# Kernel optimization log

Measured on AMD Instinct MI355X. Metric: run time of the kernel, lower is better.

Reference implementation:

```python
import jax, jax.numpy as jnp
import numpy as np

B, T, N_EMBED, HEADSIZE = 16, 2048, 1024, 128


def setup_inputs() -> dict:
    key = jax.random.key(0)
    kx, kq, kk, kv = jax.random.split(key, 4)
    x = jax.random.normal(kx, (B, T, N_EMBED), dtype=jnp.float32)
    # nn.Linear(n_embed, headsize, bias=False): y = x @ W, W stored [n_embed, headsize]
    s = (1.0 / np.sqrt(N_EMBED)).astype(np.float32)
    Wq = jax.random.normal(kq, (N_EMBED, HEADSIZE), dtype=jnp.float32) * s
    Wk = jax.random.normal(kk, (N_EMBED, HEADSIZE), dtype=jnp.float32) * s
    Wv = jax.random.normal(kv, (N_EMBED, HEADSIZE), dtype=jnp.float32) * s
    return {"x": x, "Wq": Wq, "Wk": Wk, "Wv": Wv}


def reference(x, Wq, Wk, Wv):
    Bsz, Tlen, C = x.shape
    q = x @ Wq  # [B, T, H]
    k = x @ Wk  # [B, T, H]
    v = x @ Wv  # [B, T, H]
    scale = C ** (-0.5)  # NOTE: original scales by n_embed**-0.5, not headsize**-0.5
    wt = jnp.einsum('bqh,bkh->bqk', q, k) * scale  # [B, T, T]
    causal = jnp.tril(jnp.ones((Tlen, Tlen), dtype=bool))
    wt = jnp.where(causal, wt, -jnp.inf)
    wt = jax.nn.softmax(wt, axis=-1)
    # dropout is identity in eval mode
    out = jnp.einsum('bqk,bkh->bqh', wt, v)  # [B, T, H]
    return out
```

## Files before the change

### kernel.cpp

```cpp
#include <hip/hip_runtime.h>
#include <hip/hip_bf16.h>

#define BATCH 16
#define TLEN 2048
#define CDIM 1024
#define HDIM 128

typedef __attribute__((ext_vector_type(8))) short bf16x8;
typedef __attribute__((ext_vector_type(4))) float f32x4;
typedef __attribute__((ext_vector_type(16))) float f32x16;
typedef __attribute__((ext_vector_type(4))) unsigned short u16x4;
typedef __attribute__((ext_vector_type(8))) unsigned short u16x8;

static __device__ __forceinline__ unsigned short f2bf(float f) {
    __hip_bfloat16 h = __float2bfloat16(f);
    return *(unsigned short*)&h;
}
static __device__ __forceinline__ unsigned pkbf(float a, float b) {
    return (unsigned)f2bf(a) | ((unsigned)f2bf(b) << 16);
}
static __device__ __forceinline__ int part_offs(int qc) {
    const int g = qc >> 2;
    return qc + 2 * g * (g - 1) + (qc & 3) * g;
}

typedef const __attribute__((address_space(1))) unsigned int* gas_t;
typedef __attribute__((address_space(3))) unsigned int* las_t;
static __device__ __forceinline__ void gl_lds16(const void* g, void* l) {
    __builtin_amdgcn_global_load_lds((gas_t)g, (las_t)l, 16, 0, 0);
}

static __device__ __forceinline__ void hard_barrier() {
    __builtin_amdgcn_sched_barrier(0);
    __builtin_amdgcn_s_barrier();
    __builtin_amdgcn_sched_barrier(0);
}

__global__ __launch_bounds__(256) void pack_w(
    const float* __restrict__ Wq, const float* __restrict__ Wk,
    const float* __restrict__ Wv, unsigned short* __restrict__ wtb)
{
    const int which = blockIdx.y;
    const float* W = (which == 0) ? Wq : (which == 1) ? Wk : Wv;
    const int n = blockIdx.x >> 2;
    const int k = (blockIdx.x & 3) * 256 + threadIdx.x;
    wtb[((size_t)which * 128 + n) * 1024 + k] = f2bf(W[(size_t)k * 128 + n]);
}

__global__ __launch_bounds__(512, 2) void qkv_fused(
    const float* __restrict__ x, const unsigned short* __restrict__ wtb,
    unsigned short* __restrict__ qb, unsigned short* __restrict__ kb,
    unsigned short* __restrict__ vtb)
{
    __shared__ __align__(16) unsigned short Ab[2][256 * 64];
    __shared__ __align__(16) unsigned short Bb[2][192 * 64];

    const int xcd = blockIdx.x & 7, s = blockIdx.x >> 3;
    const int m0 = (xcd * 16 + (s >> 1)) * 256;
    const int nh = s & 1;

    const int tid  = threadIdx.x;
    const int lane = tid & 63, wid = tid >> 6;
    const int wm = wid >> 2, wn = wid & 3;
    const int c = lane & 15, g = lane >> 4;

    const int arow = tid >> 1, ah = tid & 1;
    const float* xsrc = x + (size_t)(m0 + arow) * CDIM + ah * 32;

    f32x4 acc[8][3];
#pragma unroll
    for (int i = 0; i < 8; ++i)
#pragma unroll
        for (int j = 0; j < 3; ++j) acc[i][j] = (f32x4){0.f, 0.f, 0.f, 0.f};

    float4 As0, As1, As2, As3, As4, As5, As6, As7;

#define AISSUE(k0_)                                                          \
    { const float* s_ = xsrc + (k0_);                                        \
      As0 = *(const float4*)(s_);       As1 = *(const float4*)(s_ + 4);      \
      As2 = *(const float4*)(s_ + 8);   As3 = *(const float4*)(s_ + 12);     \
      As4 = *(const float4*)(s_ + 16);  As5 = *(const float4*)(s_ + 20);     \
      As6 = *(const float4*)(s_ + 24);  As7 = *(const float4*)(s_ + 28); }

#define CVT2(lo_, hi_, dst_)                                                 \
    { u16x8 t_;                                                              \
      t_[0]=f2bf(lo_.x); t_[1]=f2bf(lo_.y); t_[2]=f2bf(lo_.z); t_[3]=f2bf(lo_.w); \
      t_[4]=f2bf(hi_.x); t_[5]=f2bf(hi_.y); t_[6]=f2bf(hi_.z); t_[7]=f2bf(hi_.w); \
      *(u16x8*)(dst_) = t_; }

#define AWRITE(bi_)                                                          \
    { char* ba_ = (char*)Ab[bi_] + arow * 128;                               \
      const int sw_ = (arow & 7) << 4;                                       \
      CVT2(As0, As1, ba_ + ((ah * 64 +  0) ^ sw_));                          \
      CVT2(As2, As3, ba_ + ((ah * 64 + 16) ^ sw_));                          \
      CVT2(As4, As5, ba_ + ((ah * 64 + 32) ^ sw_));                          \
      CVT2(As6, As7, ba_ + ((ah * 64 + 48) ^ sw_)); }

#define BISSUE(k0_, bi_)                                                     \
    { _Pragma("unroll")                                                      \
      for (int i_ = 0; i_ < 3; ++i_) {                                       \
          const int seg_ = wid * 3 + i_;                                     \
          const int row_ = seg_ * 8 + (lane >> 3);                           \
          const int gr_  = (lane & 7) ^ (row_ & 7);                          \
          gl_lds16(wtb + (size_t)(nh * 192 + row_) * 1024 + (k0_) + gr_ * 8, \
                   (char*)Bb[bi_] + seg_ * 1024);                            \
      } }

    AISSUE(0);
    BISSUE(0, 0);
    asm volatile("s_waitcnt vmcnt(3)" ::: "memory");
    AWRITE(0);
    asm volatile("s_waitcnt vmcnt(0) lgkmcnt(0)" ::: "memory");
    hard_barrier();

#pragma unroll 1
    for (int kt = 0; kt < 16; ++kt) {
        const int cur = kt & 1;
        if (kt < 15) {
            AISSUE((kt + 1) * 64);
            BISSUE((kt + 1) * 64, cur ^ 1);
        }

#pragma unroll
        for (int ks = 0; ks < 2; ++ks) {
            bf16x8 af[8], bf[3];
#pragma unroll
            for (int mf = 0; mf < 8; ++mf) {
                const int rm = wm * 128 + mf * 16 + c;
                af[mf] = *(const bf16x8*)((char*)Ab[cur] + rm * 128 +
                                          ((ks * 64 + g * 16) ^ ((rm & 7) << 4)));
            }
#pragma unroll
            for (int nf = 0; nf < 3; ++nf) {
                const int rn = wn * 48 + nf * 16 + c;
                bf[nf] = *(const bf16x8*)((char*)Bb[cur] + rn * 128 +
                                          ((ks * 64 + g * 16) ^ ((rn & 7) << 4)));
            }
            __builtin_amdgcn_s_setprio(1);
#pragma unroll
            for (int mf = 0; mf < 8; ++mf)
#pragma unroll
                for (int nf = 0; nf < 3; ++nf)
                    acc[mf][nf] = __builtin_amdgcn_mfma_f32_16x16x32_bf16(
                        af[mf], bf[nf], acc[mf][nf], 0, 0, 0);
            __builtin_amdgcn_s_setprio(0);
        }

        if (kt < 15) {
            asm volatile("s_waitcnt vmcnt(3)" ::: "memory");
            AWRITE(cur ^ 1);
            asm volatile("s_waitcnt vmcnt(0) lgkmcnt(0)" ::: "memory");
            hard_barrier();
        }
    }

#pragma unroll
    for (int mf = 0; mf < 8; ++mf) {
#pragma unroll
        for (int nf = 0; nf < 3; ++nf) {
            const int col0 = nh * 192 + wn * 48 + nf * 16;
            const int nt = col0 >> 7;
            const int nc = (col0 & 127) + c;
            const int m = m0 + wm * 128 + mf * 16 + g * 4;
            if (nt == 0) {
#pragma unroll
                for (int r = 0; r < 4; ++r)
                    qb[(size_t)(m + r) * HDIM + nc] = f2bf(acc[mf][nf][r] * 0.03125f);
            } else if (nt == 1) {
#pragma unroll
                for (int r = 0; r < 4; ++r)
                    kb[(size_t)(m + r) * HDIM + nc] = f2bf(acc[mf][nf][r]);
            } else {
                const int b = m >> 11, tl = m & (TLEN - 1);
                u16x4 o;
                o[0] = f2bf(acc[mf][nf][0]); o[1] = f2bf(acc[mf][nf][1]);
                o[2] = f2bf(acc[mf][nf][2]); o[3] = f2bf(acc[mf][nf][3]);
                *(u16x4*)(vtb + ((size_t)b * HDIM + nc) * TLEN + tl) = o;
            }
        }
    }
#undef AISSUE
#undef CVT2
#undef AWRITE
#undef BISSUE
}

__global__ __launch_bounds__(256, 2) void attn_partial(
    const short* __restrict__ qb, const short* __restrict__ kb,
    const short* __restrict__ vtb,
    unsigned short* __restrict__ Opart, float* __restrict__ mpart,
    float* __restrict__ lpart)
{
    const int kc = blockIdx.x;
    const int qc = blockIdx.y;
    const int b  = blockIdx.z;
    if (kc > (qc >> 2)) return;
    const int kv_base = kc * 512;
    const int qrel = qc * 128 - kv_base;
    int NT = (qrel >> 6) + 2; if (NT > 8) NT = 8;

    __shared__ unsigned short Ks[2][64 * 128];
    __shared__ unsigned short Vs[2][128 * 64];

    const int tid  = threadIdx.x;
    const int wid  = tid >> 6;
    const int lane = tid & 63;
    const int c5 = lane & 31, hi = lane >> 5;
    const int q0w = qc * 128 + wid * 32;
    const int qg  = q0w + c5;
    const int pidx = b * 40 + part_offs(qc) + kc;

    const short* Kb  = kb  + (size_t)b * TLEN * HDIM;
    const short* Vtb = vtb + (size_t)b * HDIM * TLEN;

    bf16x8 qf[8];
#pragma unroll
    for (int ks = 0; ks < 8; ++ks)
        qf[ks] = *(const bf16x8*)(qb + ((size_t)b * TLEN + qg) * HDIM + ks * 16 + hi * 8);

    bf16x8 kst[4], vst[4];

#define GLOAD(kv0_)                                                          \
    {                                                                        \
        _Pragma("unroll")                                                    \
        for (int it = 0; it < 4; ++it) {                                     \
            const int o = tid * 16 + it * 4096;                              \
            const int kr = o >> 8, kcb = o & 0xF0;                           \
            kst[it] = *(const bf16x8*)((const char*)Kb +                     \
                        (size_t)((kv0_) + kr) * 256 + kcb);                  \
            const int vr = o >> 7, vcb = o & 0x70;                           \
            vst[it] = *(const bf16x8*)((const char*)Vtb +                    \
                        (size_t)vr * (TLEN * 2) + (size_t)(kv0_) * 2 + vcb); \
        }                                                                    \
    }
#define SSTORE(bi_)                                                          \
    {                                                                        \
        _Pragma("unroll")                                                    \
        for (int it = 0; it < 4; ++it) {                                     \
            const int o = tid * 16 + it * 4096;                              \
            const int kr = o >> 8, kcb = o & 0xF0;                           \
            *(bf16x8*)((char*)Ks[bi_] + kr * 256 + (kcb ^ ((kr & 7) << 4))) = kst[it]; \
            const int vr = o >> 7, vcb = o & 0x70;                           \
            *(bf16x8*)((char*)Vs[bi_] + vr * 128 + (vcb ^ ((vr & 7) << 4))) = vst[it]; \
        }                                                                    \
    }

    GLOAD(kv_base);
    SSTORE(0);
    __syncthreads();

    f32x16 oacc[4];
#pragma unroll
    for (int i = 0; i < 4; ++i)
#pragma unroll
        for (int r = 0; r < 16; ++r) oacc[i][r] = 0.f;
    float m_r = -1e30f;
    float l_r = 0.f;

#pragma unroll 1
    for (int t = 0; t < NT; ++t) {
        const int bi = t & 1;
        if (t + 1 < NT) GLOAD(kv_base + 64 * (t + 1));

        const int kv0 = kv_base + 64 * t;
        if (kv0 <= q0w + 31) {
            f32x16 s0, s1;
#pragma unroll
            for (int r = 0; r < 16; ++r) { s0[r] = 0.f; s1[r] = 0.f; }
            __builtin_amdgcn_s_setprio(1);
#pragma unroll
            for (int ks = 0; ks < 8; ++ks) {
                const int col = ks * 32 + hi * 16;
                const int off0 = c5 * 256 + (col ^ ((c5 & 7) << 4));
                const int off1 = (32 + c5) * 256 + (col ^ ((c5 & 7) << 4));
                bf16x8 a0 = *(const bf16x8*)((char*)Ks[bi] + off0);
                bf16x8 a1 = *(const bf16x8*)((char*)Ks[bi] + off1);
                s0 = __builtin_amdgcn_mfma_f32_32x32x16_bf16(a0, qf[ks], s0, 0, 0, 0);
                s1 = __builtin_amdgcn_mfma_f32_32x32x16_bf16(a1, qf[ks], s1, 0, 0, 0);
            }
            __builtin_amdgcn_s_setprio(0);

            if (kv0 + 63 > q0w) {
#pragma unroll
                for (int r = 0; r < 16; ++r) {
                    const int key0 = kv0 + (r & 3) + 8 * (r >> 2) + 4 * hi;
                    if (key0 > qg)      s0[r] = -INFINITY;
                    if (key0 + 32 > qg) s1[r] = -INFINITY;
                }
            }

            float t8[8];
#pragma unroll
            for (int i = 0; i < 8; ++i)
                t8[i] = fmaxf(fmaxf(s0[2*i], s0[2*i+1]), fmaxf(s1[2*i], s1[2*i+1]));
            float smax = fmaxf(fmaxf(fmaxf(t8[0], t8[1]), fmaxf(t8[2], t8[3])),
                               fmaxf(fmaxf(t8[4], t8[5]), fmaxf(t8[6], t8[7])));
            smax = fmaxf(smax, __shfl_xor(smax, 32));

            const bool defer = __all(smax - m_r <= 8.0f);
            const float mnew = defer ? m_r : fmaxf(m_r, smax);
            if (!defer) {
                const float alpha = __expf(m_r - mnew);
                l_r *= alpha;
#pragma unroll
                for (int hb = 0; hb < 4; ++hb) oacc[hb] = oacc[hb] * alpha;
            }
            m_r = mnew;

#pragma unroll
            for (int r = 0; r < 16; ++r) {
                s0[r] = __expf(s0[r] - mnew);
                s1[r] = __expf(s1[r] - mnew);
            }
            float a8[8];
#pragma unroll
            for (int i = 0; i < 8; ++i)
                a8[i] = (s0[2*i] + s0[2*i+1]) + (s1[2*i] + s1[2*i+1]);
            float psum = ((a8[0] + a8[1]) + (a8[2] + a8[3])) +
                         ((a8[4] + a8[5]) + (a8[6] + a8[7]));
            psum += __shfl_xor(psum, 32);
            l_r += psum;

            bf16x8 pa[4];
#pragma unroll
            for (int kb2 = 0; kb2 < 2; ++kb2) {
#pragma unroll
                for (int par = 0; par < 2; ++par) {
                    const int e = par * 8;
                    float v0, v1, v2, v3, v4, v5, v6, v7;
                    if (kb2 == 0) {
                        v0=s0[e+0]; v1=s0[e+1]; v2=s0[e+2]; v3=s0[e+3];
                        v4=s0[e+4]; v5=s0[e+5]; v6=s0[e+6]; v7=s0[e+7];
                    } else {
                        v0=s1[e+0]; v1=s1[e+1]; v2=s1[e+2]; v3=s1[e+3];
                        v4=s1[e+4]; v5=s1[e+5]; v6=s1[e+6]; v7=s1[e+7];
                    }
                    const unsigned w0 = pkbf(v0, v1), w1 = pkbf(v2, v3);
                    const unsigned w2 = pkbf(v4, v5), w3 = pkbf(v6, v7);
                    const unsigned X0 = hi ? w0 : w2;
                    const unsigned X1 = hi ? w1 : w3;
                    const unsigned R0 = (unsigned)__shfl_xor((int)X0, 32);
                    const unsigned R1 = (unsigned)__shfl_xor((int)X1, 32);
                    union { unsigned w[4]; bf16x8 v; } uu;
                    uu.w[0] = hi ? R0 : w0;  uu.w[1] = hi ? R1 : w1;
                    uu.w[2] = hi ? w2 : R0;  uu.w[3] = hi ? w3 : R1;
                    pa[kb2 * 2 + par] = uu.v;
                }
            }

            __builtin_amdgcn_s_setprio(1);
#pragma unroll
            for (int hb = 0; hb < 4; ++hb) {
                const int row = hb * 32 + c5;
#pragma unroll
                for (int ks = 0; ks < 4; ++ks) {
                    const int off = row * 128 + ((ks * 32 + hi * 16) ^ ((row & 7) << 4));
                    bf16x8 va = *(const bf16x8*)((char*)Vs[bi] + off);
                    oacc[hb] = __builtin_amdgcn_mfma_f32_32x32x16_bf16(va, pa[ks], oacc[hb], 0, 0, 0);
                }
            }
            __builtin_amdgcn_s_setprio(0);
        }

        if (t + 1 < NT) {
            SSTORE(bi ^ 1);
            __syncthreads();
        }
    }

    __syncthreads();
    char* sl = (char*)Ks + wid * 8192;
#pragma unroll
    for (int hb = 0; hb < 4; ++hb)
#pragma unroll
        for (int rq = 0; rq < 4; ++rq) {
            u16x4 o4;
            o4[0] = f2bf(oacc[hb][rq * 4 + 0]);
            o4[1] = f2bf(oacc[hb][rq * 4 + 1]);
            o4[2] = f2bf(oacc[hb][rq * 4 + 2]);
            o4[3] = f2bf(oacc[hb][rq * 4 + 3]);
            const int off = c5 * 256 + ((hb * 64 + rq * 16 + hi * 8) ^ ((c5 & 7) << 4));
            *(u16x4*)(sl + off) = o4;
        }
    asm volatile("s_waitcnt lgkmcnt(0)" ::: "memory");
    __builtin_amdgcn_sched_barrier(0);

    const int qr = lane >> 1, hf = lane & 1;
    unsigned short* Og = Opart + (size_t)pidx * 128 * 128 +
                         (size_t)(wid * 32 + qr) * 128 + hf * 64;
#pragma unroll
    for (int i = 0; i < 8; ++i) {
        const int off = qr * 256 + ((hf * 128 + i * 16) ^ ((qr & 7) << 4));
        *(u16x8*)(Og + i * 8) = *(const u16x8*)(sl + off);
    }
    if (hi == 0) {
        mpart[(size_t)pidx * 128 + wid * 32 + c5] = m_r;
        lpart[(size_t)pidx * 128 + wid * 32 + c5] = l_r;
    }
#undef GLOAD
#undef SSTORE
}

__global__ __launch_bounds__(256) void attn_combine(
    const unsigned short* __restrict__ Opart, const float* __restrict__ mpart,
    const float* __restrict__ lpart, float* __restrict__ out)
{
    const int qc = blockIdx.x;
    const int b  = blockIdx.y;
    const int n  = (qc >> 2) + 1;
    const int base = b * 40 + part_offs(qc);
    const int t   = threadIdx.x;
    const int row = t >> 1;
    const int d0  = (t & 1) * 64;

    float mv[4], lv[4];
#pragma unroll
    for (int p = 0; p < 4; ++p) {
        mv[p] = (p < n) ? mpart[(size_t)(base + p) * 128 + row] : -INFINITY;
        lv[p] = (p < n) ? lpart[(size_t)(base + p) * 128 + row] : 0.f;
    }
    float M = fmaxf(fmaxf(mv[0], mv[1]), fmaxf(mv[2], mv[3]));
    float L = 0.f;
    float wv[4];
#pragma unroll
    for (int p = 0; p < 4; ++p) {
        wv[p] = (p < n) ? __expf(mv[p] - M) : 0.f;
        L += wv[p] * lv[p];
    }

    float acc[64];
#pragma unroll
    for (int i = 0; i < 64; ++i) acc[i] = 0.f;

    for (int p = 0; p < n; ++p) {
        const float w = wv[p];
        const bf16x8* src = (const bf16x8*)(Opart +
            ((size_t)(base + p) * 128 + row) * 128 + d0);
#pragma unroll
        for (int j = 0; j < 8; ++j) {
            bf16x8 v = src[j];
#pragma unroll
            for (int e = 0; e < 8; ++e) {
                union { unsigned u; float f; } xx;
                xx.u = ((unsigned)(unsigned short)v[e]) << 16;
                acc[j * 8 + e] += w * xx.f;
            }
        }
    }

    const float invL = 1.f / L;
    float4* dst = (float4*)(out + ((size_t)(b * TLEN + qc * 128 + row)) * 128 + d0);
#pragma unroll
    for (int i = 0; i < 16; ++i)
        dst[i] = make_float4(acc[4*i] * invL, acc[4*i+1] * invL,
                             acc[4*i+2] * invL, acc[4*i+3] * invL);
}

extern "C" void kernel_launch(void* const* d_in, const int* in_sizes, int n_in,
                              void* d_out, int out_size, void* d_ws, size_t ws_size,
                              hipStream_t stream)
{
    const float* x  = (const float*)d_in[0];
    const float* Wq = (const float*)d_in[1];
    const float* Wk = (const float*)d_in[2];
    const float* Wv = (const float*)d_in[3];
    float* outp = (float*)d_out;

    const size_t per = (size_t)BATCH * TLEN * HDIM;
    unsigned short* qb  = (unsigned short*)d_ws;
    unsigned short* kb  = qb + per;
    unsigned short* vtb = kb + per;
    unsigned short* wtb = vtb + per;
    unsigned short* Opart = wtb + 384 * 1024;
    float* mpart = (float*)(Opart + (size_t)640 * 128 * 128);
    float* lpart = mpart + (size_t)640 * 128;

    dim3 gw(512, 3);
    pack_w<<<gw, 256, 0, stream>>>(Wq, Wk, Wv, wtb);

    qkv_fused<<<256, 512, 0, stream>>>(x, wtb, qb, kb, vtb);

    dim3 g2(4, 16, BATCH);
    attn_partial<<<g2, 256, 0, stream>>>((const short*)qb, (const short*)kb,
                                         (const short*)vtb, Opart, mpart, lpart);

    dim3 g3(16, BATCH);
    attn_combine<<<g3, 256, 0, stream>>>(Opart, mpart, lpart, outp);
}
```

Before: 136.8 us.

## Retile QKV GEMM to 128-row blocks with 32x32 MFMA and LDS-transposed weight pack

The QKV projection kernel now uses 256-thread blocks covering 128 rows instead of 512-thread blocks covering 256 rows, doubling the grid to 512 blocks. Each wave computes a 64x96 tile with 32x32x16 bf16 MFMAs instead of 16x16x32, which needs fewer fragment loads per FLOP. The weight pack kernel transposes through LDS with coalesced float4 reads and 16-byte writes instead of strided scalar accesses. Smaller M tiles mean each block reloads the weight tile for less reused work, and the epilogue issues more scattered stores.

```diff
diff --git a/kernel.cpp b/kernel.cpp
--- a/kernel.cpp
+++ b/kernel.cpp
@@ -42,36 +42,61 @@
 {
     const int which = blockIdx.y;
     const float* W = (which == 0) ? Wq : (which == 1) ? Wk : Wv;
-    const int n = blockIdx.x >> 2;
-    const int k = (blockIdx.x & 3) * 256 + threadIdx.x;
-    wtb[((size_t)which * 128 + n) * 1024 + k] = f2bf(W[(size_t)k * 128 + n]);
-}
-
-__global__ __launch_bounds__(512, 2) void qkv_fused(
+    const int k0 = blockIdx.x * 64;
+
+    __shared__ float T[64][132];
+
+    const int tid = threadIdx.x;
+#pragma unroll
+    for (int i = 0; i < 8; ++i) {
+        const int e = tid + i * 256;
+        const int row = e >> 5, c4 = e & 31;
+        float4 v = *(const float4*)(W + (size_t)(k0 + row) * 128 + c4 * 4);
+        T[row][c4 * 4 + 0] = v.x; T[row][c4 * 4 + 1] = v.y;
+        T[row][c4 * 4 + 2] = v.z; T[row][c4 * 4 + 3] = v.w;
+    }
+    __syncthreads();
+
+    const int n  = tid >> 1;
+    const int kh = (tid & 1) * 32;
+    unsigned short* dst = wtb + ((size_t)which * 128 + n) * 1024 + k0 + kh;
+#pragma unroll
+    for (int j = 0; j < 4; ++j) {
+        u16x8 o;
+#pragma unroll
+        for (int e2 = 0; e2 < 8; ++e2)
+            o[e2] = f2bf(T[kh + j * 8 + e2][n]);
+        *(u16x8*)(dst + j * 8) = o;
+    }
+}
+
+__global__ __launch_bounds__(256, 2) void qkv_fused(
     const float* __restrict__ x, const unsigned short* __restrict__ wtb,
     unsigned short* __restrict__ qb, unsigned short* __restrict__ kb,
     unsigned short* __restrict__ vtb)
 {
-    __shared__ __align__(16) unsigned short Ab[2][256 * 64];
+    __shared__ __align__(16) unsigned short Ab[2][128 * 64];
     __shared__ __align__(16) unsigned short Bb[2][192 * 64];
 
     const int xcd = blockIdx.x & 7, s = blockIdx.x >> 3;
-    const int m0 = (xcd * 16 + (s >> 1)) * 256;
+    const int m0 = (xcd * 32 + (s >> 1)) * 128;
     const int nh = s & 1;
 
     const int tid  = threadIdx.x;
     const int lane = tid & 63, wid = tid >> 6;
-    const int wm = wid >> 2, wn = wid & 3;
-    const int c = lane & 15, g = lane >> 4;
+    const int wm = wid >> 1, wn = wid & 1;
+    const int c5 = lane & 31, hi = lane >> 5;
 
     const int arow = tid >> 1, ah = tid & 1;
     const float* xsrc = x + (size_t)(m0 + arow) * CDIM + ah * 32;
 
-    f32x4 acc[8][3];
-#pragma unroll
-    for (int i = 0; i < 8; ++i)
-#pragma unroll
-        for (int j = 0; j < 3; ++j) acc[i][j] = (f32x4){0.f, 0.f, 0.f, 0.f};
+    f32x16 acc[2][3];
+#pragma unroll
+    for (int i = 0; i < 2; ++i)
+#pragma unroll
+        for (int j = 0; j < 3; ++j)
+#pragma unroll
+            for (int r = 0; r < 16; ++r) acc[i][j][r] = 0.f;
 
     float4 As0, As1, As2, As3, As4, As5, As6, As7;
 
@@ -98,8 +123,8 @@
 
 #define BISSUE(k0_, bi_)                                                     \
     { _Pragma("unroll")                                                      \
-      for (int i_ = 0; i_ < 3; ++i_) {                                       \
-          const int seg_ = wid * 3 + i_;                                     \
+      for (int i_ = 0; i_ < 6; ++i_) {                                       \
+          const int seg_ = wid * 6 + i_;                                     \
           const int row_ = seg_ * 8 + (lane >> 3);                           \
           const int gr_  = (lane & 7) ^ (row_ & 7);                          \
           gl_lds16(wtb + (size_t)(nh * 192 + row_) * 1024 + (k0_) + gr_ * 8, \
@@ -108,7 +133,7 @@
 
     AISSUE(0);
     BISSUE(0, 0);
-    asm volatile("s_waitcnt vmcnt(3)" ::: "memory");
+    asm volatile("s_waitcnt vmcnt(6)" ::: "memory");
     AWRITE(0);
     asm volatile("s_waitcnt vmcnt(0) lgkmcnt(0)" ::: "memory");
     hard_barrier();
@@ -122,32 +147,32 @@
         }
 
 #pragma unroll
-        for (int ks = 0; ks < 2; ++ks) {
-            bf16x8 af[8], bf[3];
-#pragma unroll
-            for (int mf = 0; mf < 8; ++mf) {
-                const int rm = wm * 128 + mf * 16 + c;
-                af[mf] = *(const bf16x8*)((char*)Ab[cur] + rm * 128 +
-                                          ((ks * 64 + g * 16) ^ ((rm & 7) << 4)));
-            }
-#pragma unroll
-            for (int nf = 0; nf < 3; ++nf) {
-                const int rn = wn * 48 + nf * 16 + c;
-                bf[nf] = *(const bf16x8*)((char*)Bb[cur] + rn * 128 +
-                                          ((ks * 64 + g * 16) ^ ((rn & 7) << 4)));
+        for (int kk = 0; kk < 4; ++kk) {
+            bf16x8 af[2], bf[3];
+#pragma unroll
+            for (int tm = 0; tm < 2; ++tm) {
+                const int rm = wm * 64 + tm * 32 + c5;
+                af[tm] = *(const bf16x8*)((char*)Ab[cur] + rm * 128 +
+                                          ((kk * 32 + hi * 16) ^ ((rm & 7) << 4)));
+            }
+#pragma unroll
+            for (int tn = 0; tn < 3; ++tn) {
+                const int rn = wn * 96 + tn * 32 + c5;
+                bf[tn] = *(const bf16x8*)((char*)Bb[cur] + rn * 128 +
+                                          ((kk * 32 + hi * 16) ^ ((rn & 7) << 4)));
             }
             __builtin_amdgcn_s_setprio(1);
 #pragma unroll
-            for (int mf = 0; mf < 8; ++mf)
-#pragma unroll
-                for (int nf = 0; nf < 3; ++nf)
-                    acc[mf][nf] = __builtin_amdgcn_mfma_f32_16x16x32_bf16(
-                        af[mf], bf[nf], acc[mf][nf], 0, 0, 0);
+            for (int tm = 0; tm < 2; ++tm)
+#pragma unroll
+                for (int tn = 0; tn < 3; ++tn)
+                    acc[tm][tn] = __builtin_amdgcn_mfma_f32_32x32x16_bf16(
+                        af[tm], bf[tn], acc[tm][tn], 0, 0, 0);
             __builtin_amdgcn_s_setprio(0);
         }
 
         if (kt < 15) {
-            asm volatile("s_waitcnt vmcnt(3)" ::: "memory");
+            asm volatile("s_waitcnt vmcnt(6)" ::: "memory");
             AWRITE(cur ^ 1);
             asm volatile("s_waitcnt vmcnt(0) lgkmcnt(0)" ::: "memory");
             hard_barrier();
@@ -155,27 +180,39 @@
     }
 
 #pragma unroll
-    for (int mf = 0; mf < 8; ++mf) {
-#pragma unroll
-        for (int nf = 0; nf < 3; ++nf) {
-            const int col0 = nh * 192 + wn * 48 + nf * 16;
-            const int nt = col0 >> 7;
-            const int nc = (col0 & 127) + c;
-            const int m = m0 + wm * 128 + mf * 16 + g * 4;
+    for (int tm = 0; tm < 2; ++tm) {
+#pragma unroll
+        for (int tn = 0; tn < 3; ++tn) {
+            const int colg = nh * 192 + wn * 96 + tn * 32;
+            const int nt = colg >> 7;
+            const int nc = (colg & 127) + c5;
+            const int mb2 = m0 + wm * 64 + tm * 32 + 4 * hi;
             if (nt == 0) {
 #pragma unroll
-                for (int r = 0; r < 4; ++r)
-                    qb[(size_t)(m + r) * HDIM + nc] = f2bf(acc[mf][nf][r] * 0.03125f);
+                for (int j = 0; j < 4; ++j)
+#pragma unroll
+                    for (int rr = 0; rr < 4; ++rr)
+                        qb[(size_t)(mb2 + 8 * j + rr) * HDIM + nc] =
+                            f2bf(acc[tm][tn][j * 4 + rr] * 0.03125f);
             } else if (nt == 1) {
 #pragma unroll
-                for (int r = 0; r < 4; ++r)
-                    kb[(size_t)(m + r) * HDIM + nc] = f2bf(acc[mf][nf][r]);
+                for (int j = 0; j < 4; ++j)
+#pragma unroll
+                    for (int rr = 0; rr < 4; ++rr)
+                        kb[(size_t)(mb2 + 8 * j + rr) * HDIM + nc] =
+                            f2bf(acc[tm][tn][j * 4 + rr]);
             } else {
-                const int b = m >> 11, tl = m & (TLEN - 1);
-                u16x4 o;
-                o[0] = f2bf(acc[mf][nf][0]); o[1] = f2bf(acc[mf][nf][1]);
-                o[2] = f2bf(acc[mf][nf][2]); o[3] = f2bf(acc[mf][nf][3]);
-                *(u16x4*)(vtb + ((size_t)b * HDIM + nc) * TLEN + tl) = o;
+#pragma unroll
+                for (int j = 0; j < 4; ++j) {
+                    const int m = mb2 + 8 * j;
+                    const int b = m >> 11, tl = m & (TLEN - 1);
+                    u16x4 o;
+                    o[0] = f2bf(acc[tm][tn][j * 4 + 0]);
+                    o[1] = f2bf(acc[tm][tn][j * 4 + 1]);
+                    o[2] = f2bf(acc[tm][tn][j * 4 + 2]);
+                    o[3] = f2bf(acc[tm][tn][j * 4 + 3]);
+                    *(u16x4*)(vtb + ((size_t)b * HDIM + nc) * TLEN + tl) = o;
+                }
             }
         }
     }
@@ -475,10 +512,10 @@
     float* mpart = (float*)(Opart + (size_t)640 * 128 * 128);
     float* lpart = mpart + (size_t)640 * 128;
 
-    dim3 gw(512, 3);
+    dim3 gw(16, 3);
     pack_w<<<gw, 256, 0, stream>>>(Wq, Wk, Wv, wtb);
 
-    qkv_fused<<<256, 512, 0, stream>>>(x, wtb, qb, kb, vtb);
+    qkv_fused<<<512, 256, 0, stream>>>(x, wtb, qb, kb, vtb);
 
     dim3 g2(4, 16, BATCH);
     attn_partial<<<g2, 256, 0, stream>>>((const short*)qb, (const short*)kb,
```

Measured after the change: 134.2 us. About the same (-1.9%).
